# Performance work log

Measured on AMD Instinct MI355X. Metric: run time of the kernel, lower is better.

Reference implementation:

```python
import jax, jax.numpy as jnp
import numpy as np

B, N, D, H, NW = 16, 400, 256, 8, 4
DH = D // H
EPS_LN = 1e-5

def _layer_norm(x, g, b):
    m = jnp.mean(x, axis=-1, keepdims=True)
    v = jnp.mean((x - m) ** 2, axis=-1, keepdims=True)
    return (x - m) / jnp.sqrt(v + EPS_LN) * g + b

def setup_inputs() -> dict:
    key = jax.random.key(0)
    ks = jax.random.split(key, 10)
    p = lambda k, shape: (jax.random.normal(k, shape, jnp.float32) * 0.02)
    return {
        'x': jax.random.normal(ks[0], (B, N, D), jnp.float32),
        'attention_weights': jax.random.normal(ks[1], (B, NW, N, N), jnp.float32),
        'Wq': p(ks[2], (D, D)), 'bq': jnp.zeros((D,), jnp.float32),
        'Wk': p(ks[3], (D, D)), 'bk': jnp.zeros((D,), jnp.float32),
        'Wv': p(ks[4], (D, D)), 'bv': jnp.zeros((D,), jnp.float32),
        'Wo': p(ks[5], (D, D)), 'bo': jnp.zeros((D,), jnp.float32),
        'g1': jnp.ones((D,), jnp.float32), 'beta1': jnp.zeros((D,), jnp.float32),
        'W1': p(ks[6], (4 * D, D)), 'b1': jnp.zeros((4 * D,), jnp.float32),
        'W2': p(ks[7], (D, 4 * D)), 'b2': jnp.zeros((D,), jnp.float32),
        'g2': jnp.ones((D,), jnp.float32), 'beta2': jnp.zeros((D,), jnp.float32),
    }

def reference(x, attention_weights, Wq, bq, Wk, bk, Wv, bv, Wo, bo,
              g1, beta1, W1, b1, W2, b2, g2, beta2):
    b, n, d = x.shape
    # QKV projections, split heads: [B, H, N, DH]
    q = (x @ Wq.T + bq).reshape(b, n, H, DH).transpose(0, 2, 1, 3)
    k = (x @ Wk.T + bk).reshape(b, n, H, DH).transpose(0, 2, 1, 3)
    v = (x @ Wv.T + bv).reshape(b, n, H, DH).transpose(0, 2, 1, 3)
    qk = jnp.einsum('bhnd,bhmd->bhnm', q, k) / np.sqrt(DH)  # [B,H,N,N]
    # signed attention averaged over the NW per-sample weight matrices
    nw = attention_weights.shape[1]
    scores = jnp.zeros_like(qk)
    for i in range(nw):  # small fixed count, not a data dim
        w = attention_weights[:, i][:, None, :, :]  # [B,1,N,N]
        s = qk * w
        e = jnp.exp(jnp.abs(s))
        scores = scores + jnp.sign(s) * e / (jnp.sum(e, axis=-1, keepdims=True) + 1e-10)
    scores = scores / nw
    attn_out = jnp.einsum('bhnm,bhmd->bhnd', scores, v)
    attn_out = attn_out.transpose(0, 2, 1, 3).reshape(b, n, d)
    attn_out = attn_out @ Wo.T + bo
    h = _layer_norm(x + attn_out, g1, beta1)
    ffn = jax.nn.relu(h @ W1.T + b1) @ W2.T + b2
    y = _layer_norm(h + ffn, g2, beta2)
    return (y, scores)
```

## Files before the change

### kernel.cpp

```cpp
#include <hip/hip_runtime.h>
#include <hip/hip_fp16.h>

typedef unsigned int uint32;

#define B_ 16
#define N_ 400
#define D_ 256
#define H_ 8
#define DH_ 32
#define NW_ 4

#if __has_builtin(__builtin_amdgcn_exp2f)
#define EXP2(x) __builtin_amdgcn_exp2f(x)
#else
#define EXP2(x) exp2f(x)
#endif

#define QK_SCL 0.2550348f

using bf16x8 = __attribute__((ext_vector_type(8))) short;
using f16x8  = __attribute__((ext_vector_type(8))) _Float16;
using f16x4  = __attribute__((ext_vector_type(4))) _Float16;
using f32x4  = __attribute__((ext_vector_type(4))) float;

__device__ __forceinline__ ushort f2b(float f) {
  uint32 u = __float_as_uint(f);
  uint32 r = (u + 0x7fffu + ((u >> 16) & 1u)) >> 16;
  return (ushort)r;
}

__global__ __launch_bounds__(256) void convert_kernel(
    const float* __restrict__ x,  const float* __restrict__ wq,
    const float* __restrict__ wk, const float* __restrict__ wv,
    const float* __restrict__ wo, const float* __restrict__ w1,
    const float* __restrict__ w2,
    ushort* __restrict__ xb,  ushort* __restrict__ wqb,
    ushort* __restrict__ wkb, ushort* __restrict__ wvb,
    ushort* __restrict__ wob, ushort* __restrict__ w1b,
    ushort* __restrict__ w2b) {
  int gid = blockIdx.x * 256 + threadIdx.x;
  const float* src; ushort* dst;
  if      (gid < 409600) { src = x;  dst = xb;  }
  else if ((gid -= 409600) < 16384) { src = wq; dst = wqb; }
  else if ((gid -= 16384) < 16384)  { src = wk; dst = wkb; }
  else if ((gid -= 16384) < 16384)  { src = wv; dst = wvb; }
  else if ((gid -= 16384) < 16384)  { src = wo; dst = wob; }
  else if ((gid -= 16384) < 65536)  { src = w1; dst = w1b; }
  else { gid -= 65536; src = w2; dst = w2b; }
  float4 f = ((const float4*)src)[gid];
  ushort4 u;
  u.x = f2b(f.x); u.y = f2b(f.y); u.z = f2b(f.z); u.w = f2b(f.w);
  *(ushort4*)&dst[(size_t)gid * 4] = u;
}

template <int RELU, int RESID, int OUT_F32, int OUT_BF16>
__global__ __launch_bounds__(256) void gemm_bt(
    const ushort* __restrict__ A, const ushort* __restrict__ W,
    const float* __restrict__ bias, const float* __restrict__ resid,
    float* __restrict__ outf, ushort* __restrict__ outb,
    int M, int N, int K) {
  __shared__ __align__(16) ushort As[2][64 * 40];
  __shared__ __align__(16) ushort Ws[2][64 * 40];
  int t = threadIdx.x;
  int l = t & 63, w = t >> 6;
  int n0 = blockIdx.x * 64, m0 = blockIdx.y * 64;
  int srow = t >> 2, sc = (t & 3) * 8;
  int lrow = l & 15, lk = (l >> 4) * 8;

  const uint4* ag = (const uint4*)&A[(size_t)(m0 + srow) * K + sc];
  const uint4* wg = (const uint4*)&W[(size_t)(n0 + srow) * K + sc];
  uint4 ar = ag[0], wr = wg[0];
  int nk = K >> 5;

  f32x4 acc[4];
#pragma unroll
  for (int nt = 0; nt < 4; nt++) acc[nt] = {0.f, 0.f, 0.f, 0.f};

  for (int kk = 0; kk < nk; kk++) {
    int cur = kk & 1;
    *(uint4*)&As[cur][srow * 40 + sc] = ar;
    *(uint4*)&Ws[cur][srow * 40 + sc] = wr;
    if (kk + 1 < nk) { ar = ag[(size_t)(kk + 1) * 4]; wr = wg[(size_t)(kk + 1) * 4]; }
    __syncthreads();
    bf16x8 af = *(const bf16x8*)&As[cur][(16 * w + lrow) * 40 + lk];
#pragma unroll
    for (int nt = 0; nt < 4; nt++) {
      bf16x8 bf = *(const bf16x8*)&Ws[cur][(nt * 16 + lrow) * 40 + lk];
      acc[nt] = __builtin_amdgcn_mfma_f32_16x16x32_bf16(af, bf, acc[nt], 0, 0, 0);
    }
  }

#pragma unroll
  for (int nt = 0; nt < 4; nt++) {
    int n = n0 + nt * 16 + lrow;
    float bv = bias[n];
#pragma unroll
    for (int r = 0; r < 4; r++) {
      int m = m0 + 16 * w + (l >> 4) * 4 + r;
      float v = acc[nt][r] + bv;
      if (RELU)  v = fmaxf(v, 0.f);
      if (RESID) v += resid[(size_t)m * N + n];
      if (OUT_F32)  outf[(size_t)m * N + n] = v;
      if (OUT_BF16) outb[(size_t)m * N + n] = f2b(v);
    }
  }
}

__global__ __launch_bounds__(256) void qkv_gemm(
    const ushort* __restrict__ xb, const ushort* __restrict__ wq,
    const ushort* __restrict__ wk, const ushort* __restrict__ wv,
    const float* __restrict__ bq, const float* __restrict__ bk,
    const float* __restrict__ bv,
    _Float16* __restrict__ qh, _Float16* __restrict__ kh,
    _Float16* __restrict__ vt) {
  __shared__ __align__(16) ushort As[2][64 * 40];
  __shared__ __align__(16) ushort Ws[2][64 * 40];
  int z = blockIdx.z;
  const ushort* W = (z == 0) ? wq : (z == 1) ? wk : wv;
  const float* bias = (z == 0) ? bq : (z == 1) ? bk : bv;

  int t = threadIdx.x;
  int l = t & 63, w = t >> 6;
  int n0 = blockIdx.x * 64, m0 = blockIdx.y * 64;
  int srow = t >> 2, sc = (t & 3) * 8;
  int lrow = l & 15, lk = (l >> 4) * 8;

  const uint4* ag = (const uint4*)&xb[(size_t)(m0 + srow) * 256 + sc];
  const uint4* wg = (const uint4*)&W[(size_t)(n0 + srow) * 256 + sc];
  uint4 ar = ag[0], wr = wg[0];

  f32x4 acc[4];
#pragma unroll
  for (int nt = 0; nt < 4; nt++) acc[nt] = {0.f, 0.f, 0.f, 0.f};

  for (int kk = 0; kk < 8; kk++) {
    int cur = kk & 1;
    *(uint4*)&As[cur][srow * 40 + sc] = ar;
    *(uint4*)&Ws[cur][srow * 40 + sc] = wr;
    if (kk + 1 < 8) { ar = ag[(kk + 1) * 4]; wr = wg[(kk + 1) * 4]; }
    __syncthreads();
    bf16x8 af = *(const bf16x8*)&As[cur][(16 * w + lrow) * 40 + lk];
#pragma unroll
    for (int nt = 0; nt < 4; nt++) {
      bf16x8 bf = *(const bf16x8*)&Ws[cur][(nt * 16 + lrow) * 40 + lk];
      acc[nt] = __builtin_amdgcn_mfma_f32_16x16x32_bf16(af, bf, acc[nt], 0, 0, 0);
    }
  }

  int mb = m0 + 16 * w + (l >> 4) * 4;
  int bb = mb / 400;
  int mi = mb - bb * 400;
#pragma unroll
  for (int nt = 0; nt < 4; nt++) {
    int n = n0 + nt * 16 + lrow;
    float bvv = bias[n];
    if (z < 2) {
      _Float16* out = z ? kh : qh;
      float scl = z ? 1.f : QK_SCL;
      int hh = n >> 5, dd = n & 31;
      _Float16* dst = out + (((size_t)(bb * 8 + hh)) * 400 + mi) * 32 + dd;
#pragma unroll
      for (int r = 0; r < 4; r++)
        dst[(size_t)r * 32] = (_Float16)((acc[nt][r] + bvv) * scl);
    } else {
      _Float16 h4[4];
#pragma unroll
      for (int r = 0; r < 4; r++) h4[r] = (_Float16)(acc[nt][r] + bvv);
      *(uint2*)&vt[((size_t)bb * 256 + n) * 400 + mi] = *(uint2*)h4;
    }
  }
}

#define SP 416

__global__ __launch_bounds__(256, 8) void attn_kernel(
    const _Float16* __restrict__ qh, const _Float16* __restrict__ kh,
    const _Float16* __restrict__ vt, const float* __restrict__ aw,
    float* __restrict__ scores, ushort* __restrict__ attnb) {
  __shared__ __align__(16) char smem[16 * SP * 2];
  __half* S = (__half*)smem;

  int id = blockIdx.x;
  int c = ((id >> 6) << 3) | (id & 7);
  int hh = (id >> 3) & 7;
  int b = c / 25;
  int n0 = (c - b * 25) * 16;

  int t = threadIdx.x;
  int w = t >> 6, l = t & 63;
  int lq = l >> 4, lr = l & 15;

  {
    const _Float16* qbase = qh + (((size_t)(b * 8 + hh)) * 400 + n0) * 32;
    const _Float16* kbase = kh + ((size_t)(b * 8 + hh)) * 400 * 32;
    f16x8 af = *(const f16x8*)(qbase + lr * 32 + lq * 8);
    for (int mt = w; mt < 25; mt += 4) {
      f16x8 bf = *(const f16x8*)(kbase + (size_t)(mt * 16 + lr) * 32 + lq * 8);
      f32x4 cc = {0.f, 0.f, 0.f, 0.f};
      cc = __builtin_amdgcn_mfma_f32_16x16x32_f16(af, bf, cc, 0, 0, 0);
#pragma unroll
      for (int r = 0; r < 4; r++)
        S[(lq * 4 + r) * SP + mt * 16 + lr] = __float2half(cc[r]);
    }
  }
  __syncthreads();

  {
    int m0 = l * 4, m1 = 256 + l * 4;
    bool act = (l < 36);
    const float* awb = aw + (((size_t)(b * 4)) * 400 + n0) * 400;
    float* scb = scores + (((size_t)(b * 8 + hh)) * 400 + n0) * 400;
#pragma unroll 1
    for (int g = 0; g < 4; g++) {
      int n = g * 4 + w;
      _Float16* srow = (_Float16*)S + (size_t)n * SP;
      const float* awn = awb + (size_t)n * 400;
      float* scout = scb + (size_t)n * 400;

      f16x4 s0 = *(const f16x4*)(srow + m0);
      float q0[4], q1[4];
#pragma unroll
      for (int j = 0; j < 4; j++) q0[j] = (float)s0[j];
      if (act) {
        f16x4 s1 = *(const f16x4*)(srow + m1);
#pragma unroll
        for (int j = 0; j < 4; j++) q1[j] = (float)s1[j];
      } else {
#pragma unroll
        for (int j = 0; j < 4; j++) q1[j] = 0.f;
      }

      f16x4 e0[4], e1[4];
      float z[4];
#pragma unroll
      for (int i = 0; i < 4; i++) {
        const float* awi = awn + (size_t)i * 160000;
        float4 a0 = *(const float4*)(awi + m0);
        float zz = 0.f;
#pragma unroll
        for (int j = 0; j < 4; j++) {
          float tt = q0[j] * ((const float*)&a0)[j];
          float ef = EXP2(fabsf(tt));
          zz += ef;
          e0[i][j] = (_Float16)copysignf(ef, tt);
        }
        if (act) {
          float4 a1 = *(const float4*)(awi + m1);
#pragma unroll
          for (int j = 0; j < 4; j++) {
            float tt = q1[j] * ((const float*)&a1)[j];
            float ef = EXP2(fabsf(tt));
            zz += ef;
            e1[i][j] = (_Float16)copysignf(ef, tt);
          }
        } else {
#pragma unroll
          for (int j = 0; j < 4; j++) e1[i][j] = (_Float16)0.f;
        }
        z[i] = zz;
      }

#pragma unroll
      for (int o = 1; o <= 32; o <<= 1) {
#pragma unroll
        for (int i = 0; i < 4; i++) z[i] += __shfl_xor(z[i], o);
      }

      f16x4 o0, o1;
#pragma unroll
      for (int j = 0; j < 4; j++) { o0[j] = (_Float16)0.f; o1[j] = (_Float16)0.f; }
#pragma unroll
      for (int i = 0; i < 4; i++) {
        _Float16 zh = (_Float16)(0.25f / (z[i] + 1e-10f));
        f16x4 zv = {zh, zh, zh, zh};
        o0 += e0[i] * zv;
        o1 += e1[i] * zv;
      }

      float4 so;
#pragma unroll
      for (int j = 0; j < 4; j++) ((float*)&so)[j] = (float)o0[j];
      *(float4*)(scout + m0) = so;
      *(f16x4*)(srow + m0) = o0;
      if (act) {
        float4 s1o;
#pragma unroll
        for (int j = 0; j < 4; j++) ((float*)&s1o)[j] = (float)o1[j];
        *(float4*)(scout + m1) = s1o;
        *(f16x4*)(srow + m1) = o1;
      } else if (l < 40) {
        f16x4 hz;
#pragma unroll
        for (int j = 0; j < 4; j++) hz[j] = (_Float16)0.f;
        *(f16x4*)(srow + m1) = hz;
      }
    }
  }
  __syncthreads();

  const _Float16* vbase = vt + (((size_t)b) * 256 + hh * 32) * 400;
  f32x4 a0 = {0.f, 0.f, 0.f, 0.f}, a1 = {0.f, 0.f, 0.f, 0.f};
  const _Float16* Sh = (const _Float16*)S;
  for (int c2 = w; c2 < 13; c2 += 4) {
    f16x8 sf = *(const f16x8*)(Sh + lr * SP + c2 * 32 + lq * 8);
    f16x8 v0 = *(const f16x8*)(vbase + (size_t)lr * 400 + c2 * 32 + lq * 8);
    f16x8 v1 = *(const f16x8*)(vbase + (size_t)(16 + lr) * 400 + c2 * 32 + lq * 8);
    a0 = __builtin_amdgcn_mfma_f32_16x16x32_f16(sf, v0, a0, 0, 0, 0);
    a1 = __builtin_amdgcn_mfma_f32_16x16x32_f16(sf, v1, a1, 0, 0, 0);
  }
  __syncthreads();
  float* Of = (float*)smem;
#pragma unroll
  for (int r = 0; r < 4; r++) {
    Of[(w * 16 + lq * 4 + r) * 32 + lr] = a0[r];
    Of[(w * 16 + lq * 4 + r) * 32 + 16 + lr] = a1[r];
  }
  __syncthreads();
  for (int o = t; o < 512; o += 256) {
    int n = o >> 5, d = o & 31;
    float s = Of[n * 32 + d] + Of[512 + n * 32 + d] +
              Of[1024 + n * 32 + d] + Of[1536 + n * 32 + d];
    attnb[((size_t)(b * 400 + n0 + n)) * 256 + hh * 32 + d] = f2b(s);
  }
}

__global__ __launch_bounds__(256) void ln_kernel(
    const float* __restrict__ src, const float* __restrict__ g,
    const float* __restrict__ be, float* __restrict__ outf,
    ushort* __restrict__ outb) {
  int row = blockIdx.x, t = threadIdx.x;
  float v = src[(size_t)row * 256 + t];
  __shared__ float red[4];
  float s = v;
#pragma unroll
  for (int o = 32; o > 0; o >>= 1) s += __shfl_down(s, o, 64);
  if ((t & 63) == 0) red[t >> 6] = s;
  __syncthreads();
  float mean = (red[0] + red[1] + red[2] + red[3]) * (1.f / 256.f);
  __syncthreads();
  float d = v - mean;
  s = d * d;
#pragma unroll
  for (int o = 32; o > 0; o >>= 1) s += __shfl_down(s, o, 64);
  if ((t & 63) == 0) red[t >> 6] = s;
  __syncthreads();
  float var = (red[0] + red[1] + red[2] + red[3]) * (1.f / 256.f);
  float y = d * rsqrtf(var + 1e-5f) * g[t] + be[t];
  outf[(size_t)row * 256 + t] = y;
  if (outb) outb[(size_t)row * 256 + t] = f2b(y);
}

extern "C" void kernel_launch(void* const* d_in, const int* in_sizes, int n_in,
                              void* d_out, int out_size, void* d_ws,
                              size_t ws_size, hipStream_t stream) {
  const float* x   = (const float*)d_in[0];
  const float* aw  = (const float*)d_in[1];
  const float* Wq  = (const float*)d_in[2];
  const float* bq  = (const float*)d_in[3];
  const float* Wk  = (const float*)d_in[4];
  const float* bk  = (const float*)d_in[5];
  const float* Wv  = (const float*)d_in[6];
  const float* bv  = (const float*)d_in[7];
  const float* Wo  = (const float*)d_in[8];
  const float* bo  = (const float*)d_in[9];
  const float* g1  = (const float*)d_in[10];
  const float* be1 = (const float*)d_in[11];
  const float* W1  = (const float*)d_in[12];
  const float* b1  = (const float*)d_in[13];
  const float* W2  = (const float*)d_in[14];
  const float* b2  = (const float*)d_in[15];
  const float* g2  = (const float*)d_in[16];
  const float* be2 = (const float*)d_in[17];

  if (ws_size < 34340864) return;

  char* ws = (char*)d_ws;
  ushort*   xb    = (ushort*)(ws + 0);
  ushort*   wqb   = (ushort*)(ws + 3276800);
  ushort*   wkb   = (ushort*)(ws + 3407872);
  ushort*   wvb   = (ushort*)(ws + 3538944);
  ushort*   wob   = (ushort*)(ws + 3670016);
  ushort*   w1b   = (ushort*)(ws + 3801088);
  ushort*   w2b   = (ushort*)(ws + 4325376);
  _Float16* qhb   = (_Float16*)(ws + 4849664);
  _Float16* khb   = (_Float16*)(ws + 8126464);
  _Float16* vtb   = (_Float16*)(ws + 11403264);
  ushort*   attnb = (ushort*)(ws + 14680064);
  float*    ao    = (float*)(ws + 17956864);
  float*    hbuf  = (float*)(ws + 24510464);
  ushort*   hb    = (ushort*)(ws + 31064064);
  ushort*   ffn1b = (ushort*)qhb;
  float*    ffn2  = ao;

  float* yout   = (float*)d_out;
  float* scores = yout + 1638400;

  convert_kernel<<<2368, 256, 0, stream>>>(x, Wq, Wk, Wv, Wo, W1, W2,
                                           xb, wqb, wkb, wvb, wob, w1b, w2b);
  qkv_gemm<<<dim3(4, 100, 3), 256, 0, stream>>>(
      xb, wqb, wkb, wvb, bq, bk, bv, qhb, khb, vtb);
  attn_kernel<<<3200, 256, 0, stream>>>(qhb, khb, vtb, aw, scores, attnb);
  gemm_bt<0, 1, 1, 0><<<dim3(4, 100), 256, 0, stream>>>(
      attnb, wob, bo, x, ao, nullptr, 6400, 256, 256);
  ln_kernel<<<6400, 256, 0, stream>>>(ao, g1, be1, hbuf, hb);
  gemm_bt<1, 0, 0, 1><<<dim3(16, 100), 256, 0, stream>>>(
      hb, w1b, b1, nullptr, nullptr, ffn1b, 6400, 1024, 256);
  gemm_bt<0, 1, 1, 0><<<dim3(4, 100), 256, 0, stream>>>(
      ffn1b, w2b, b2, hbuf, ffn2, nullptr, 6400, 256, 1024);
  ln_kernel<<<6400, 256, 0, stream>>>(ffn2, g2, be2, yout, nullptr);
}
```

Measured before the change: 276.1 us.

## Process four heads per attention block to reuse attention_weights loads

```diff
diff --git a/kernel.cpp b/kernel.cpp
--- a/kernel.cpp
+++ b/kernel.cpp
@@ -173,154 +173,198 @@
 
 #define SP 416
 
-__global__ __launch_bounds__(256, 8) void attn_kernel(
+__global__ __launch_bounds__(256, 3) void attn_kernel(
     const _Float16* __restrict__ qh, const _Float16* __restrict__ kh,
     const _Float16* __restrict__ vt, const float* __restrict__ aw,
     float* __restrict__ scores, ushort* __restrict__ attnb) {
-  __shared__ __align__(16) char smem[16 * SP * 2];
-  __half* S = (__half*)smem;
+  __shared__ __align__(16) __half S[4][16][SP];
 
   int id = blockIdx.x;
-  int c = ((id >> 6) << 3) | (id & 7);
-  int hh = (id >> 3) & 7;
+  int c = ((id >> 4) << 3) | (id & 7);
+  int hg = (id >> 3) & 1;
   int b = c / 25;
   int n0 = (c - b * 25) * 16;
+  int h0 = hg * 4;
 
   int t = threadIdx.x;
   int w = t >> 6, l = t & 63;
   int lq = l >> 4, lr = l & 15;
 
   {
-    const _Float16* qbase = qh + (((size_t)(b * 8 + hh)) * 400 + n0) * 32;
-    const _Float16* kbase = kh + ((size_t)(b * 8 + hh)) * 400 * 32;
-    f16x8 af = *(const f16x8*)(qbase + lr * 32 + lq * 8);
+    const size_t bh8 = (size_t)b * 8 + h0;
+    f16x8 af[4];
+#pragma unroll
+    for (int h = 0; h < 4; h++)
+      af[h] = *(const f16x8*)(qh + ((bh8 + h) * 400 + n0 + lr) * 32 + lq * 8);
     for (int mt = w; mt < 25; mt += 4) {
-      f16x8 bf = *(const f16x8*)(kbase + (size_t)(mt * 16 + lr) * 32 + lq * 8);
-      f32x4 cc = {0.f, 0.f, 0.f, 0.f};
-      cc = __builtin_amdgcn_mfma_f32_16x16x32_f16(af, bf, cc, 0, 0, 0);
-#pragma unroll
-      for (int r = 0; r < 4; r++)
-        S[(lq * 4 + r) * SP + mt * 16 + lr] = __float2half(cc[r]);
+      f16x8 bf[4];
+#pragma unroll
+      for (int h = 0; h < 4; h++)
+        bf[h] = *(const f16x8*)(kh + ((bh8 + h) * 400 + mt * 16 + lr) * 32 + lq * 8);
+#pragma unroll
+      for (int h = 0; h < 4; h++) {
+        f32x4 cc = {0.f, 0.f, 0.f, 0.f};
+        cc = __builtin_amdgcn_mfma_f32_16x16x32_f16(af[h], bf[h], cc, 0, 0, 0);
+#pragma unroll
+        for (int r = 0; r < 4; r++)
+          S[h][lq * 4 + r][mt * 16 + lr] = __float2half(cc[r]);
+      }
     }
   }
   __syncthreads();
 
   {
+    const float* awb = aw + (((size_t)(b * 4)) * 400 + n0) * 400;
+    float* scb = scores + (((size_t)(b * 8 + h0)) * 400 + n0) * 400;
     int m0 = l * 4, m1 = 256 + l * 4;
     bool act = (l < 36);
-    const float* awb = aw + (((size_t)(b * 4)) * 400 + n0) * 400;
-    float* scb = scores + (((size_t)(b * 8 + hh)) * 400 + n0) * 400;
+
+    float4 zf4 = {0.f, 0.f, 0.f, 0.f};
+    float4 cA0[4] = {zf4, zf4, zf4, zf4};
+    float4 cA1[4] = {zf4, zf4, zf4, zf4};
+    float4 nA0[4] = {zf4, zf4, zf4, zf4};
+    float4 nA1[4] = {zf4, zf4, zf4, zf4};
+    {
+      const float* awn = awb + (size_t)w * 400;
+#pragma unroll
+      for (int i = 0; i < 4; i++)
+        cA0[i] = *(const float4*)(awn + (size_t)i * 160000 + m0);
+      if (act) {
+#pragma unroll
+        for (int i = 0; i < 4; i++)
+          cA1[i] = *(const float4*)(awn + (size_t)i * 160000 + m1);
+      }
+    }
+
 #pragma unroll 1
     for (int g = 0; g < 4; g++) {
       int n = g * 4 + w;
-      _Float16* srow = (_Float16*)S + (size_t)n * SP;
-      const float* awn = awb + (size_t)n * 400;
-      float* scout = scb + (size_t)n * 400;
-
-      f16x4 s0 = *(const f16x4*)(srow + m0);
-      float q0[4], q1[4];
-#pragma unroll
-      for (int j = 0; j < 4; j++) q0[j] = (float)s0[j];
-      if (act) {
-        f16x4 s1 = *(const f16x4*)(srow + m1);
-#pragma unroll
-        for (int j = 0; j < 4; j++) q1[j] = (float)s1[j];
-      } else {
-#pragma unroll
-        for (int j = 0; j < 4; j++) q1[j] = 0.f;
-      }
-
-      f16x4 e0[4], e1[4];
-      float z[4];
-#pragma unroll
-      for (int i = 0; i < 4; i++) {
-        const float* awi = awn + (size_t)i * 160000;
-        float4 a0 = *(const float4*)(awi + m0);
-        float zz = 0.f;
-#pragma unroll
-        for (int j = 0; j < 4; j++) {
-          float tt = q0[j] * ((const float*)&a0)[j];
-          float ef = EXP2(fabsf(tt));
-          zz += ef;
-          e0[i][j] = (_Float16)copysignf(ef, tt);
+      f16x4 sh0[4], sh1[4];
+#pragma unroll
+      for (int h = 0; h < 4; h++) sh0[h] = *(const f16x4*)&S[h][n][m0];
+#pragma unroll
+      for (int h = 0; h < 4; h++)
+        sh1[h] = act ? *(const f16x4*)&S[h][n][m1]
+                     : f16x4{(_Float16)0.f, (_Float16)0.f,
+                             (_Float16)0.f, (_Float16)0.f};
+
+      float z[4][4];
+#pragma unroll
+      for (int h = 0; h < 4; h++) {
+        float q0f[4], q1f[4];
+#pragma unroll
+        for (int j = 0; j < 4; j++) q0f[j] = (float)sh0[h][j];
+#pragma unroll
+        for (int j = 0; j < 4; j++) q1f[j] = (float)sh1[h][j];
+#pragma unroll
+        for (int i = 0; i < 4; i++) {
+          float zz = 0.f;
+#pragma unroll
+          for (int j = 0; j < 4; j++)
+            zz += EXP2(fabsf(q0f[j] * ((const float*)&cA0[i])[j]));
+          if (act) {
+#pragma unroll
+            for (int j = 0; j < 4; j++)
+              zz += EXP2(fabsf(q1f[j] * ((const float*)&cA1[i])[j]));
+          }
+          z[h][i] = zz;
         }
+      }
+
+      if (g < 3) {
+        const float* awn = awb + (size_t)(n + 4) * 400;
+#pragma unroll
+        for (int i = 0; i < 4; i++)
+          nA0[i] = *(const float4*)(awn + (size_t)i * 160000 + m0);
         if (act) {
-          float4 a1 = *(const float4*)(awi + m1);
+#pragma unroll
+          for (int i = 0; i < 4; i++)
+            nA1[i] = *(const float4*)(awn + (size_t)i * 160000 + m1);
+        }
+      }
+
+#pragma unroll
+      for (int o = 1; o <= 32; o <<= 1)
+#pragma unroll
+        for (int h = 0; h < 4; h++)
+#pragma unroll
+          for (int i = 0; i < 4; i++)
+            z[h][i] += __shfl_xor(z[h][i], o);
+
+#pragma unroll
+      for (int h = 0; h < 4; h++) {
+        float zinv[4];
+#pragma unroll
+        for (int i = 0; i < 4; i++) zinv[i] = 0.25f / (z[h][i] + 1e-10f);
+        float q0f[4];
+#pragma unroll
+        for (int j = 0; j < 4; j++) q0f[j] = (float)sh0[h][j];
+        float o0[4] = {0.f, 0.f, 0.f, 0.f};
+#pragma unroll
+        for (int i = 0; i < 4; i++)
 #pragma unroll
           for (int j = 0; j < 4; j++) {
-            float tt = q1[j] * ((const float*)&a1)[j];
-            float ef = EXP2(fabsf(tt));
-            zz += ef;
-            e1[i][j] = (_Float16)copysignf(ef, tt);
+            float tt = q0f[j] * ((const float*)&cA0[i])[j];
+            o0[j] += copysignf(EXP2(fabsf(tt)) * zinv[i], tt);
           }
-        } else {
-#pragma unroll
-          for (int j = 0; j < 4; j++) e1[i][j] = (_Float16)0.f;
+        float* scout = scb + (size_t)h * 160000 + (size_t)n * 400;
+        float4 ov = {o0[0], o0[1], o0[2], o0[3]};
+        *(float4*)(scout + m0) = ov;
+        f16x4 hv;
+#pragma unroll
+        for (int j = 0; j < 4; j++) hv[j] = (_Float16)o0[j];
+        *(f16x4*)&S[h][n][m0] = hv;
+        if (act) {
+          float q1f[4];
+#pragma unroll
+          for (int j = 0; j < 4; j++) q1f[j] = (float)sh1[h][j];
+          float o1[4] = {0.f, 0.f, 0.f, 0.f};
+#pragma unroll
+          for (int i = 0; i < 4; i++)
+#pragma unroll
+            for (int j = 0; j < 4; j++) {
+              float tt = q1f[j] * ((const float*)&cA1[i])[j];
+              o1[j] += copysignf(EXP2(fabsf(tt)) * zinv[i], tt);
+            }
+          float4 ov1 = {o1[0], o1[1], o1[2], o1[3]};
+          *(float4*)(scout + m1) = ov1;
+          f16x4 hv1;
+#pragma unroll
+          for (int j = 0; j < 4; j++) hv1[j] = (_Float16)o1[j];
+          *(f16x4*)&S[h][n][m1] = hv1;
+        } else if (l < 40) {
+          f16x4 hz;
+#pragma unroll
+          for (int j = 0; j < 4; j++) hz[j] = (_Float16)0.f;
+          *(f16x4*)&S[h][n][m1] = hz;
         }
-        z[i] = zz;
-      }
-
-#pragma unroll
-      for (int o = 1; o <= 32; o <<= 1) {
-#pragma unroll
-        for (int i = 0; i < 4; i++) z[i] += __shfl_xor(z[i], o);
-      }
-
-      f16x4 o0, o1;
-#pragma unroll
-      for (int j = 0; j < 4; j++) { o0[j] = (_Float16)0.f; o1[j] = (_Float16)0.f; }
-#pragma unroll
-      for (int i = 0; i < 4; i++) {
-        _Float16 zh = (_Float16)(0.25f / (z[i] + 1e-10f));
-        f16x4 zv = {zh, zh, zh, zh};
-        o0 += e0[i] * zv;
-        o1 += e1[i] * zv;
-      }
-
-      float4 so;
-#pragma unroll
-      for (int j = 0; j < 4; j++) ((float*)&so)[j] = (float)o0[j];
-      *(float4*)(scout + m0) = so;
-      *(f16x4*)(srow + m0) = o0;
-      if (act) {
-        float4 s1o;
-#pragma unroll
-        for (int j = 0; j < 4; j++) ((float*)&s1o)[j] = (float)o1[j];
-        *(float4*)(scout + m1) = s1o;
-        *(f16x4*)(srow + m1) = o1;
-      } else if (l < 40) {
-        f16x4 hz;
-#pragma unroll
-        for (int j = 0; j < 4; j++) hz[j] = (_Float16)0.f;
-        *(f16x4*)(srow + m1) = hz;
+      }
+
+      if (g < 3) {
+#pragma unroll
+        for (int i = 0; i < 4; i++) { cA0[i] = nA0[i]; cA1[i] = nA1[i]; }
       }
     }
   }
   __syncthreads();
 
-  const _Float16* vbase = vt + (((size_t)b) * 256 + hh * 32) * 400;
-  f32x4 a0 = {0.f, 0.f, 0.f, 0.f}, a1 = {0.f, 0.f, 0.f, 0.f};
-  const _Float16* Sh = (const _Float16*)S;
-  for (int c2 = w; c2 < 13; c2 += 4) {
-    f16x8 sf = *(const f16x8*)(Sh + lr * SP + c2 * 32 + lq * 8);
-    f16x8 v0 = *(const f16x8*)(vbase + (size_t)lr * 400 + c2 * 32 + lq * 8);
-    f16x8 v1 = *(const f16x8*)(vbase + (size_t)(16 + lr) * 400 + c2 * 32 + lq * 8);
-    a0 = __builtin_amdgcn_mfma_f32_16x16x32_f16(sf, v0, a0, 0, 0, 0);
-    a1 = __builtin_amdgcn_mfma_f32_16x16x32_f16(sf, v1, a1, 0, 0, 0);
-  }
-  __syncthreads();
-  float* Of = (float*)smem;
-#pragma unroll
-  for (int r = 0; r < 4; r++) {
-    Of[(w * 16 + lq * 4 + r) * 32 + lr] = a0[r];
-    Of[(w * 16 + lq * 4 + r) * 32 + 16 + lr] = a1[r];
-  }
-  __syncthreads();
-  for (int o = t; o < 512; o += 256) {
-    int n = o >> 5, d = o & 31;
-    float s = Of[n * 32 + d] + Of[512 + n * 32 + d] +
-              Of[1024 + n * 32 + d] + Of[1536 + n * 32 + d];
-    attnb[((size_t)(b * 400 + n0 + n)) * 256 + hh * 32 + d] = f2b(s);
+  {
+    const _Float16* vbase = vt + (((size_t)b) * 256 + (h0 + w) * 32) * 400;
+    const _Float16* Sh = (const _Float16*)&S[w][0][0];
+    f32x4 a0 = {0.f, 0.f, 0.f, 0.f}, a1 = {0.f, 0.f, 0.f, 0.f};
+    for (int c2 = 0; c2 < 13; c2++) {
+      f16x8 sf = *(const f16x8*)(Sh + lr * SP + c2 * 32 + lq * 8);
+      f16x8 v0 = *(const f16x8*)(vbase + (size_t)lr * 400 + c2 * 32 + lq * 8);
+      f16x8 v1 = *(const f16x8*)(vbase + (size_t)(16 + lr) * 400 + c2 * 32 + lq * 8);
+      a0 = __builtin_amdgcn_mfma_f32_16x16x32_f16(sf, v0, a0, 0, 0, 0);
+      a1 = __builtin_amdgcn_mfma_f32_16x16x32_f16(sf, v1, a1, 0, 0, 0);
+    }
+#pragma unroll
+    for (int r = 0; r < 4; r++) {
+      size_t row = (size_t)(b * 400 + n0 + lq * 4 + r);
+      attnb[row * 256 + (h0 + w) * 32 + lr]      = f2b(a0[r]);
+      attnb[row * 256 + (h0 + w) * 32 + 16 + lr] = f2b(a1[r]);
+    }
   }
 }
 
@@ -399,7 +443,7 @@
                                            xb, wqb, wkb, wvb, wob, w1b, w2b);
   qkv_gemm<<<dim3(4, 100, 3), 256, 0, stream>>>(
       xb, wqb, wkb, wvb, bq, bk, bv, qhb, khb, vtb);
-  attn_kernel<<<3200, 256, 0, stream>>>(qhb, khb, vtb, aw, scores, attnb);
+  attn_kernel<<<800, 256, 0, stream>>>(qhb, khb, vtb, aw, scores, attnb);
   gemm_bt<0, 1, 1, 0><<<dim3(4, 100), 256, 0, stream>>>(
       attnb, wob, bo, x, ao, nullptr, 6400, 256, 256);
   ln_kernel<<<6400, 256, 0, stream>>>(ao, g1, be1, hbuf, hb);
```

Result: slower. 391.2 us (+41.7%).
